# Kernel tuning notes

Hardware: AMD Instinct MI355X
Metric: run time of the kernel (lower is better)

Reference implementation:

```python
import jax, jax.numpy as jnp
import numpy as np

N_NODES = 100000
N_EDGES = 1600000
D_FEAT = 128
HIDDEN = 64
N_CLASSES = 40
NEG_SLOPE = 0.01  # jax.nn.leaky_relu default, matches flax nn.leaky_relu


def glorot(key, shape):
    fan_in, fan_out = shape
    return jax.random.normal(key, shape, dtype=jnp.float32) * jnp.sqrt(2.0 / (fan_in + fan_out))


def setup_inputs() -> dict:
    key = jax.random.key(0)
    ks = jax.random.split(key, 8)
    nodes = jax.random.normal(ks[0], (N_NODES, D_FEAT), dtype=jnp.float32)
    senders = jax.random.randint(ks[1], (N_EDGES,), 0, N_NODES, dtype=jnp.int32)
    receivers = jax.random.randint(ks[2], (N_EDGES,), 0, N_NODES, dtype=jnp.int32)
    W1 = glorot(ks[3], (D_FEAT, HIDDEN))
    b1 = jnp.zeros((HIDDEN,), jnp.float32)
    W2 = glorot(ks[4], (HIDDEN, HIDDEN))
    b2 = jnp.zeros((HIDDEN,), jnp.float32)
    W3 = glorot(ks[5], (HIDDEN, N_CLASSES))
    b3 = jnp.zeros((N_CLASSES,), jnp.float32)
    return {"nodes": nodes, "senders": senders, "receivers": receivers,
            "W1": W1, "b1": b1, "W2": W2, "b2": b2, "W3": W3, "b3": b3}


def gcn_aggregate(x, senders, receivers, n_nodes):
    """jraph.GraphConvolution symmetric_normalization aggregation (post update_node_fn)."""
    ones = jnp.ones(senders.shape[0], dtype=x.dtype)
    sender_deg = jax.ops.segment_sum(ones, senders, num_segments=n_nodes)
    receiver_deg = jax.ops.segment_sum(ones, receivers, num_segments=n_nodes)
    x = x * jax.lax.rsqrt(jnp.maximum(sender_deg, 1.0))[:, None]
    x = jax.ops.segment_sum(x[senders], receivers, num_segments=n_nodes)  # [N, F]
    x = x * jax.lax.rsqrt(jnp.maximum(receiver_deg, 1.0))[:, None]
    return x


def reference(nodes, senders, receivers, W1, b1, W2, b2, W3, b3):
    n = nodes.shape[0]
    # Layer 1: GraphConvolution(MLP([hidden, hidden], leaky_relu))
    h = jax.nn.leaky_relu(nodes @ W1 + b1, NEG_SLOPE)
    h = jax.nn.leaky_relu(h @ W2 + b2, NEG_SLOPE)
    h = gcn_aggregate(h, senders, receivers, n)
    # Dropout is deterministic (training=False) -> identity
    # Layer 2: GraphConvolution(Dense(number_classes))
    h = h @ W3 + b3
    h = gcn_aggregate(h, senders, receivers, n)
    return jax.nn.softmax(h, axis=-1)
```

## Files before the change

kernel.cpp:

```cpp
#include <hip/hip_runtime.h>
#include <hip/hip_fp16.h>

#define NEG_SLOPE 0.01f
#define RANGE_BITS 15
#define RANGE (1 << RANGE_BITS)
#define HWORDS (RANGE / 2)
#define SLICE_BITS 15
#define SLICE (1 << SLICE_BITS)

typedef _Float16 f16x8 __attribute__((ext_vector_type(8)));
typedef float f32x4 __attribute__((ext_vector_type(4)));

__device__ __forceinline__ float lrelu(float x) { return x > 0.f ? x : NEG_SLOPE * x; }

__device__ __forceinline__ unsigned pack2h(float a, float b) {
    __half2 h = __floats2half2_rn(a, b);
    unsigned u; __builtin_memcpy(&u, &h, 4); return u;
}
__device__ __forceinline__ float2 unpack2(unsigned u) {
    __half2 h = *reinterpret_cast<__half2*>(&u);
    return __half22float2(h);
}
__device__ __forceinline__ f16x8 u4h8(uint4 u) {
    f16x8 r; __builtin_memcpy(&r, &u, 16); return r;
}

__global__ __launch_bounds__(1024) void count_kernel(
    const int* __restrict__ snd, const int* __restrict__ rcv,
    unsigned* __restrict__ partial, unsigned short* __restrict__ pos16,
    int nE, int NR, int NS)
{
    __shared__ unsigned hist[HWORDS];
    const int b = blockIdx.x;
    const int a = b / (NR * NS);
    const int rem = b - a * NR * NS;
    const int r = rem / NS;
    const int s = rem - r * NS;
    const int t = threadIdx.x;
    for (int k = t; k < HWORDS; k += 1024) hist[k] = 0u;
    __syncthreads();
    const int base = r << RANGE_BITS;
    const int lo = s << SLICE_BITS;
    const int hi = min(lo + SLICE, nE);
    const int n4 = (hi - lo) >> 2;
    const int* arr = (a == 0) ? rcv : snd;
    const int4* arr4 = (const int4*)(arr + lo);
    if (a == 0) {
        for (int i4 = t; i4 < n4; i4 += 1024) {
            const int4 v = arr4[i4];
            const int ib = lo + i4 * 4;
            int vv[4] = {v.x, v.y, v.z, v.w};
#pragma unroll
            for (int c = 0; c < 4; ++c) {
                const unsigned d = (unsigned)(vv[c] - base);
                if (d < (unsigned)RANGE) {
                    const unsigned sh = (d & 1u) << 4;
                    const unsigned old = atomicAdd(&hist[d >> 1], 1u << sh);
                    pos16[ib + c] = (unsigned short)((old >> sh) & 0xffffu);
                }
            }
        }
        for (int i = lo + n4 * 4 + t; i < hi; i += 1024) {
            const unsigned d = (unsigned)(arr[i] - base);
            if (d < (unsigned)RANGE) {
                const unsigned sh = (d & 1u) << 4;
                const unsigned old = atomicAdd(&hist[d >> 1], 1u << sh);
                pos16[i] = (unsigned short)((old >> sh) & 0xffffu);
            }
        }
    } else {
        for (int i4 = t; i4 < n4; i4 += 1024) {
            const int4 v = arr4[i4];
            int vv[4] = {v.x, v.y, v.z, v.w};
#pragma unroll
            for (int c = 0; c < 4; ++c) {
                const unsigned d = (unsigned)(vv[c] - base);
                if (d < (unsigned)RANGE) atomicAdd(&hist[d >> 1], 1u << ((d & 1u) << 4));
            }
        }
        for (int i = lo + n4 * 4 + t; i < hi; i += 1024) {
            const unsigned d = (unsigned)(arr[i] - base);
            if (d < (unsigned)RANGE) atomicAdd(&hist[d >> 1], 1u << ((d & 1u) << 4));
        }
    }
    __syncthreads();
    unsigned* dst = partial + (size_t)((a * NR + r) * NS + s) * HWORDS;
    for (int k = t; k < HWORDS; k += 1024) dst[k] = hist[k];
}

__global__ __launch_bounds__(256) void scanp_kernel(
    unsigned* __restrict__ partial,
    int* __restrict__ dr_i,
    float* __restrict__ rin, float* __restrict__ rout,
    int nN, int NR, int NS)
{
    const int gid = blockIdx.x * 256 + threadIdx.x;
    if (gid >= NR * HWORDS) return;
    const int r  = gid >> (RANGE_BITS - 1);
    const int wd = gid & (HWORDS - 1);
    unsigned* prcv = partial + (size_t)(r * NS) * HWORDS + wd;
    unsigned run0 = 0, run1 = 0;
    for (int s = 0; s < NS; ++s) {
        unsigned* p = prcv + (size_t)s * HWORDS;
        const unsigned c = *p;
        *p = run0 | (run1 << 16);
        run0 += c & 0xffffu;
        run1 += c >> 16;
    }
    const unsigned* psnd = partial + (size_t)((NR + r) * NS) * HWORDS + wd;
    unsigned t0 = 0, t1 = 0;
    for (int s = 0; s < NS; ++s) {
        const unsigned c = psnd[(size_t)s * HWORDS];
        t0 += c & 0xffffu;
        t1 += c >> 16;
    }
    const int n0 = (r << RANGE_BITS) + 2 * wd;
    if (n0 < nN) {
        dr_i[n0] = (int)run0;
        rout[n0] = rsqrtf(fmaxf((float)run0, 1.f));
        rin[n0]  = rsqrtf(fmaxf((float)t0, 1.f));
    }
    if (n0 + 1 < nN) {
        dr_i[n0 + 1] = (int)run1;
        rout[n0 + 1] = rsqrtf(fmaxf((float)run1, 1.f));
        rin[n0 + 1]  = rsqrtf(fmaxf((float)t1, 1.f));
    }
}

__global__ __launch_bounds__(256) void scan1_kernel(const int* __restrict__ cnt,
                                                    int* __restrict__ rowptr,
                                                    int* __restrict__ bsums, int n)
{
    __shared__ int sd[256];
    const int t = threadIdx.x;
    const int base = blockIdx.x * 1024 + t * 4;
    int v0 = (base + 0 < n) ? cnt[base + 0] : 0;
    int v1 = (base + 1 < n) ? cnt[base + 1] : 0;
    int v2 = (base + 2 < n) ? cnt[base + 2] : 0;
    int v3 = (base + 3 < n) ? cnt[base + 3] : 0;
    const int p1 = v0, p2 = v0 + v1, p3 = v0 + v1 + v2;
    const int tot = p3 + v3;
    sd[t] = tot;
    __syncthreads();
    for (int off = 1; off < 256; off <<= 1) {
        int y = (t >= off) ? sd[t - off] : 0;
        __syncthreads();
        sd[t] += y;
        __syncthreads();
    }
    const int excl = sd[t] - tot;
    if (base + 0 < n) rowptr[base + 0] = excl;
    if (base + 1 < n) rowptr[base + 1] = excl + p1;
    if (base + 2 < n) rowptr[base + 2] = excl + p2;
    if (base + 3 < n) rowptr[base + 3] = excl + p3;
    if (t == 255) bsums[blockIdx.x] = sd[255];
}

__global__ __launch_bounds__(256) void scan2_kernel(int* __restrict__ bsums, int nb)
{
    __shared__ int sd[256];
    const int t = threadIdx.x;
    const int v = (t < nb) ? bsums[t] : 0;
    sd[t] = v;
    __syncthreads();
    for (int off = 1; off < 256; off <<= 1) {
        int y = (t >= off) ? sd[t - off] : 0;
        __syncthreads();
        sd[t] += y;
        __syncthreads();
    }
    if (t < nb) bsums[t] = sd[t] - v;
}

__global__ __launch_bounds__(256) void scan3_kernel(int* __restrict__ rowptr,
                                                    const int* __restrict__ bsums,
                                                    int n, int nE)
{
    const int gid = blockIdx.x * 256 + threadIdx.x;
    if (gid < n) rowptr[gid] += bsums[gid >> 10];
    if (gid == 0) rowptr[n] = nE;
}

__global__ __launch_bounds__(256) void fill_kernel(
    const int* __restrict__ snd, const int* __restrict__ rcv,
    const unsigned short* __restrict__ pos16, const unsigned* __restrict__ partial,
    const int* __restrict__ rowptr, int* __restrict__ csr_src,
    int nE, int NS)
{
    const int i = blockIdx.x * 256 + threadIdx.x;
    if (i >= nE) return;
    const int rv = rcv[i];
    const int r = rv >> RANGE_BITS;
    const int s = i >> SLICE_BITS;
    const unsigned pw = partial[(size_t)(r * NS + s) * HWORDS + ((rv & (RANGE - 1)) >> 1)];
    const int pref = (int)((pw >> ((rv & 1) << 4)) & 0xffffu);
    const int pos = rowptr[rv] + pref + (int)pos16[i];
    csr_src[pos] = snd[i];
}

__global__ __launch_bounds__(256) void mlp_kernel(
    const float* __restrict__ X, const float* __restrict__ W1, const float* __restrict__ b1,
    const float* __restrict__ W2, const float* __restrict__ b2, const float* __restrict__ W3,
    const float* __restrict__ rin, __half* __restrict__ p, int nN)
{
    __shared__ uint4 R1[1024];
    __shared__ uint4 R2[512];

    const int t    = threadIdx.x;
    const int w    = t >> 6;
    const int l    = t & 63;
    const int lrow = l & 15;
    const int lq   = l >> 4;
    const int row0 = blockIdx.x * 64;

    {
        const int c = l;
        for (int ch = 0; ch < 4; ++ch) {
            const int kc = 4 * w + ch;
            const float* wp = W1 + (kc * 8) * 64 + c;
            uint4 u;
            u.x = pack2h(wp[0],       wp[64]);
            u.y = pack2h(wp[2 * 64],  wp[3 * 64]);
            u.z = pack2h(wp[4 * 64],  wp[5 * 64]);
            u.w = pack2h(wp[6 * 64],  wp[7 * 64]);
            R1[c * 16 + (kc ^ (c & 7))] = u;
        }
    }
    __syncthreads();

    const int grow = row0 + 16 * w + lrow;
    const bool rowok = grow < nN;
    const float* xr = X + (size_t)grow * 128 + lq * 8;

    f32x4 acc1[4];
#pragma unroll
    for (int nt = 0; nt < 4; ++nt) acc1[nt] = (f32x4){0.f, 0.f, 0.f, 0.f};

#pragma unroll
    for (int ks = 0; ks < 4; ++ks) {
        float4 xa = make_float4(0.f, 0.f, 0.f, 0.f), xb = xa;
        if (rowok) {
            xa = *(const float4*)(xr + 32 * ks);
            xb = *(const float4*)(xr + 32 * ks + 4);
        }
        uint4 au;
        au.x = pack2h(xa.x, xa.y); au.y = pack2h(xa.z, xa.w);
        au.z = pack2h(xb.x, xb.y); au.w = pack2h(xb.z, xb.w);
        const f16x8 af = u4h8(au);
        const int kc = 4 * ks + lq;
#pragma unroll
        for (int nt = 0; nt < 4; ++nt) {
            const int c = 16 * nt + lrow;
            const uint4 bu = R1[c * 16 + (kc ^ (c & 7))];
            acc1[nt] = __builtin_amdgcn_mfma_f32_16x16x32_f16(af, u4h8(bu), acc1[nt], 0, 0, 0);
        }
    }
    __syncthreads();

    {
        __half* hh = (__half*)R2;
#pragma unroll
        for (int nt = 0; nt < 4; ++nt) {
            const int col = 16 * nt + lrow;
            const float bv = b1[col];
            const int ch = col >> 3, cl = col & 7;
#pragma unroll
            for (int r = 0; r < 4; ++r) {
                const int rw = 16 * w + 4 * lq + r;
                hh[rw * 64 + ((ch ^ (rw & 7)) * 8) + cl] = __float2half(lrelu(acc1[nt][r] + bv));
            }
        }
        const int c = l;
#pragma unroll
        for (int ch = 0; ch < 2; ++ch) {
            const int kc = 2 * w + ch;
            const float* wp = W2 + (kc * 8) * 64 + c;
            uint4 u;
            u.x = pack2h(wp[0],      wp[64]);
            u.y = pack2h(wp[2 * 64], wp[3 * 64]);
            u.z = pack2h(wp[4 * 64], wp[5 * 64]);
            u.w = pack2h(wp[6 * 64], wp[7 * 64]);
            R1[c * 8 + (kc ^ (c & 7))] = u;
        }
        if (c < 48) {
            const bool cv = c < 40;
#pragma unroll
            for (int ch = 0; ch < 2; ++ch) {
                const int kc = 2 * w + ch;
                const float* wp = W3 + (kc * 8) * 40 + c;
                uint4 u;
                u.x = pack2h(cv ? wp[0]      : 0.f, cv ? wp[40]     : 0.f);
                u.y = pack2h(cv ? wp[2 * 40] : 0.f, cv ? wp[3 * 40] : 0.f);
                u.z = pack2h(cv ? wp[4 * 40] : 0.f, cv ? wp[5 * 40] : 0.f);
                u.w = pack2h(cv ? wp[6 * 40] : 0.f, cv ? wp[7 * 40] : 0.f);
                R1[512 + c * 8 + (kc ^ (c & 7))] = u;
            }
        }
    }
    __syncthreads();

    f32x4 acc2[4];
#pragma unroll
    for (int nt = 0; nt < 4; ++nt) acc2[nt] = (f32x4){0.f, 0.f, 0.f, 0.f};
    {
        const int ar = 16 * w + lrow;
#pragma unroll
        for (int ks = 0; ks < 2; ++ks) {
            const int kc = 4 * ks + lq;
            const f16x8 af = u4h8(R2[ar * 8 + (kc ^ (ar & 7))]);
#pragma unroll
            for (int nt = 0; nt < 4; ++nt) {
                const int c = 16 * nt + lrow;
                const uint4 bu = R1[c * 8 + (kc ^ (c & 7))];
                acc2[nt] = __builtin_amdgcn_mfma_f32_16x16x32_f16(af, u4h8(bu), acc2[nt], 0, 0, 0);
            }
        }
    }
    __syncthreads();

    {
        __half* hh = (__half*)R2;
#pragma unroll
        for (int nt = 0; nt < 4; ++nt) {
            const int col = 16 * nt + lrow;
            const float bv = b2[col];
            const int ch = col >> 3, cl = col & 7;
#pragma unroll
            for (int r = 0; r < 4; ++r) {
                const int rw = 16 * w + 4 * lq + r;
                hh[rw * 64 + ((ch ^ (rw & 7)) * 8) + cl] = __float2half(lrelu(acc2[nt][r] + bv));
            }
        }
    }
    __syncthreads();

    f32x4 acc3[3];
#pragma unroll
    for (int nt = 0; nt < 3; ++nt) acc3[nt] = (f32x4){0.f, 0.f, 0.f, 0.f};
    {
        const int ar = 16 * w + lrow;
#pragma unroll
        for (int ks = 0; ks < 2; ++ks) {
            const int kc = 4 * ks + lq;
            const f16x8 af = u4h8(R2[ar * 8 + (kc ^ (ar & 7))]);
#pragma unroll
            for (int nt = 0; nt < 3; ++nt) {
                const int c = 16 * nt + lrow;
                const uint4 bu = R1[512 + c * 8 + (kc ^ (c & 7))];
                acc3[nt] = __builtin_amdgcn_mfma_f32_16x16x32_f16(af, u4h8(bu), acc3[nt], 0, 0, 0);
            }
        }
    }

#pragma unroll
    for (int r = 0; r < 4; ++r) {
        const int gr = row0 + 16 * w + 4 * lq + r;
        if (gr < nN) {
            const float rs = rin[gr];
            __half* pr = p + (size_t)gr * 40;
#pragma unroll
            for (int nt = 0; nt < 3; ++nt) {
                const int col = 16 * nt + lrow;
                if (col < 40) pr[col] = __float2half(acc3[nt][r] * rs);
            }
        }
    }
}

__global__ __launch_bounds__(256) void agg1_kernel(const __half* __restrict__ p,
                                                   const int* __restrict__ csr_src,
                                                   const int* __restrict__ rowptr,
                                                   const float* __restrict__ rin,
                                                   const float* __restrict__ rout,
                                                   __half* __restrict__ qbuf,
                                                   float* __restrict__ cbuf, int nN)
{
    const int gid = blockIdx.x * 256 + threadIdx.x;
    const int node = gid >> 3;
    const int j = gid & 7;
    if (node >= nN) return;
    const int beg = rowptr[node], end = rowptr[node + 1];
    const bool isch = (j < 5);
    const bool isr  = (j == 5);
    float a[8];
#pragma unroll
    for (int k = 0; k < 8; ++k) a[k] = 0.f;
    float cs = 0.f;

    for (int e = beg; e < end; e += 8) {
        int s[8];
#pragma unroll
        for (int b = 0; b < 8; ++b) {
            const int idx = e + b;
            s[b] = csr_src[idx < end ? idx : end - 1];
        }
        if (isch) {
            uint4 u[8];
#pragma unroll
            for (int b = 0; b < 8; ++b)
                u[b] = ((const uint4*)(p + (size_t)s[b] * 40))[j];
#pragma unroll
            for (int b = 0; b < 8; ++b) {
                if (e + b < end) {
                    float2 f;
                    f = unpack2(u[b].x); a[0] += f.x; a[1] += f.y;
                    f = unpack2(u[b].y); a[2] += f.x; a[3] += f.y;
                    f = unpack2(u[b].z); a[4] += f.x; a[5] += f.y;
                    f = unpack2(u[b].w); a[6] += f.x; a[7] += f.y;
                }
            }
        } else if (isr) {
            float rr[8];
#pragma unroll
            for (int b = 0; b < 8; ++b) rr[b] = rin[s[b]];
#pragma unroll
            for (int b = 0; b < 8; ++b)
                if (e + b < end) cs += rr[b];
        }
    }

    if (isch) {
        const float sc = rin[node] * rout[node];
        uint4 o;
        o.x = pack2h(a[0] * sc, a[1] * sc);
        o.y = pack2h(a[2] * sc, a[3] * sc);
        o.z = pack2h(a[4] * sc, a[5] * sc);
        o.w = pack2h(a[6] * sc, a[7] * sc);
        ((uint4*)(qbuf + (size_t)node * 40))[j] = o;
    } else if (isr) {
        cbuf[node] = cs * rout[node];
    }
}

__global__ __launch_bounds__(256) void agg2_kernel(const __half* __restrict__ qbuf,
                                                   const int* __restrict__ csr_src,
                                                   const int* __restrict__ rowptr,
                                                   const float* __restrict__ rout,
                                                   const float* __restrict__ cbuf,
                                                   const float* __restrict__ b3,
                                                   float* __restrict__ out, int nN)
{
    const int gid = blockIdx.x * 256 + threadIdx.x;
    const int node = gid >> 3;
    const int j = gid & 7;
    if (node >= nN) return;
    const int beg = rowptr[node], end = rowptr[node + 1];
    const bool isch = (j < 5);
    float a[8];
#pragma unroll
    for (int k = 0; k < 8; ++k) a[k] = 0.f;

    for (int e = beg; e < end; e += 8) {
        int s[8];
#pragma unroll
        for (int b = 0; b < 8; ++b) {
            const int idx = e + b;
            s[b] = csr_src[idx < end ? idx : end - 1];
        }
        if (isch) {
            uint4 u[8];
#pragma unroll
            for (int b = 0; b < 8; ++b)
                u[b] = ((const uint4*)(qbuf + (size_t)s[b] * 40))[j];
#pragma unroll
            for (int b = 0; b < 8; ++b) {
                if (e + b < end) {
                    float2 f;
                    f = unpack2(u[b].x); a[0] += f.x; a[1] += f.y;
                    f = unpack2(u[b].y); a[2] += f.x; a[3] += f.y;
                    f = unpack2(u[b].z); a[4] += f.x; a[5] += f.y;
                    f = unpack2(u[b].w); a[6] += f.x; a[7] += f.y;
                }
            }
        }
    }

    const float ro = rout[node];
    const float c  = cbuf[node];
    float z[8];
    float m = -1e30f, ssum = 0.f;
    if (isch) {
#pragma unroll
        for (int k = 0; k < 8; ++k) {
            z[k] = ro * a[k] + c * b3[j * 8 + k];
            m = fmaxf(m, z[k]);
        }
    }
    m = fmaxf(m, __shfl_xor(m, 1));
    m = fmaxf(m, __shfl_xor(m, 2));
    m = fmaxf(m, __shfl_xor(m, 4));
    if (isch) {
#pragma unroll
        for (int k = 0; k < 8; ++k) { z[k] = __expf(z[k] - m); ssum += z[k]; }
    }
    ssum += __shfl_xor(ssum, 1);
    ssum += __shfl_xor(ssum, 2);
    ssum += __shfl_xor(ssum, 4);
    if (isch) {
        const float inv = 1.f / ssum;
        float4* orow = (float4*)(out + (size_t)node * 40);
        orow[j * 2 + 0] = make_float4(z[0] * inv, z[1] * inv, z[2] * inv, z[3] * inv);
        orow[j * 2 + 1] = make_float4(z[4] * inv, z[5] * inv, z[6] * inv, z[7] * inv);
    }
}

extern "C" void kernel_launch(void* const* d_in, const int* in_sizes, int n_in,
                              void* d_out, int out_size, void* d_ws, size_t ws_size,
                              hipStream_t stream)
{
    const float* nodes = (const float*)d_in[0];
    const int*   snd   = (const int*)d_in[1];
    const int*   rcv   = (const int*)d_in[2];
    const float* W1    = (const float*)d_in[3];
    const float* b1    = (const float*)d_in[4];
    const float* W2    = (const float*)d_in[5];
    const float* b2    = (const float*)d_in[6];
    const float* W3    = (const float*)d_in[7];
    const float* b3    = (const float*)d_in[8];

    const int nN = in_sizes[0] / 128;
    const int nE = in_sizes[1];
    const int NR = (nN + RANGE - 1) >> RANGE_BITS;
    const int NS = (nE + SLICE - 1) >> SLICE_BITS;
    const int nb1 = (nN + 1023) / 1024;

    size_t off = 0;
    auto alloc = [&](size_t n) { size_t r = off; off += (n + 3) & ~(size_t)3; return r; };
    int*   dr_i    = (int*)d_ws + alloc(nN);
    int*   rowptr  = (int*)d_ws + alloc(nN + 1);
    int*   bsums   = (int*)d_ws + alloc(256);
    float* rin     = (float*)d_ws + alloc(nN);
    float* rout    = (float*)d_ws + alloc(nN);
    float* cbuf    = (float*)d_ws + alloc(nN);
    int*   csr_src = (int*)d_ws + alloc(nE);
    const size_t psz = (size_t)2 * NR * NS * HWORDS;
    size_t ubase = alloc(0);
    unsigned*       partial = (unsigned*)d_ws + ubase;
    unsigned short* pos16   = (unsigned short*)((unsigned*)d_ws + ubase + psz);
    __half* pbuf = (__half*)((int*)d_ws + ubase);
    __half* qbuf = pbuf + (size_t)nN * 40;

    count_kernel<<<2 * NR * NS, 1024, 0, stream>>>(snd, rcv, partial, pos16, nE, NR, NS);
    scanp_kernel<<<(NR * HWORDS + 255) / 256, 256, 0, stream>>>(partial, dr_i, rin, rout, nN, NR, NS);
    scan1_kernel<<<nb1, 256, 0, stream>>>(dr_i, rowptr, bsums, nN);
    scan2_kernel<<<1, 256, 0, stream>>>(bsums, nb1);
    scan3_kernel<<<(nN + 255) / 256, 256, 0, stream>>>(rowptr, bsums, nN, nE);
    fill_kernel<<<(nE + 255) / 256, 256, 0, stream>>>(snd, rcv, pos16, partial, rowptr, csr_src, nE, NS);
    mlp_kernel<<<(nN + 63) / 64, 256, 0, stream>>>(nodes, W1, b1, W2, b2, W3, rin, pbuf, nN);
    agg1_kernel<<<((size_t)nN * 8 + 255) / 256, 256, 0, stream>>>(pbuf, csr_src, rowptr, rin, rout, qbuf, cbuf, nN);
    agg2_kernel<<<((size_t)nN * 8 + 255) / 256, 256, 0, stream>>>(qbuf, csr_src, rowptr, rout, cbuf, b3, (float*)d_out, nN);
}
```

Baseline: 172.5 us.

## Split second aggregation into feature-column passes with a separate softmax kernel

The layer-2 gather is split into three passes, each reading a narrower column slice of the fp16 feature table (16, 16 and 8 halves per node). Each slice is small enough to stay resident in cache, which should improve hit rates on the random gathers. Partial logits go to an fp32 staging buffer and a new per-node softmax kernel reads them back. The cost is rereading the CSR indices three times, extra launches, and extra global traffic for the staging buffer. SLICE_BITS also changes from 15 to 16, which alters the partitioning of the degree-count and CSR-build kernels.

After: 195.8 us. +13.5%, slower.

```diff
diff --git a/kernel.cpp b/kernel.cpp
--- a/kernel.cpp
+++ b/kernel.cpp
@@ -5,7 +5,7 @@
 #define RANGE_BITS 15
 #define RANGE (1 << RANGE_BITS)
 #define HWORDS (RANGE / 2)
-#define SLICE_BITS 15
+#define SLICE_BITS 16
 #define SLICE (1 << SLICE_BITS)
 
 typedef _Float16 f16x8 __attribute__((ext_vector_type(8)));
@@ -372,7 +372,9 @@
                                                    const int* __restrict__ rowptr,
                                                    const float* __restrict__ rin,
                                                    const float* __restrict__ rout,
-                                                   __half* __restrict__ qbuf,
+                                                   __half* __restrict__ qA,
+                                                   __half* __restrict__ qB,
+                                                   __half* __restrict__ qC,
                                                    float* __restrict__ cbuf, int nN)
 {
     const int gid = blockIdx.x * 256 + threadIdx.x;
@@ -426,26 +428,29 @@
         o.y = pack2h(a[2] * sc, a[3] * sc);
         o.z = pack2h(a[4] * sc, a[5] * sc);
         o.w = pack2h(a[6] * sc, a[7] * sc);
-        ((uint4*)(qbuf + (size_t)node * 40))[j] = o;
+        if (j < 2)      ((uint4*)qA)[(size_t)node * 2 + j] = o;
+        else if (j < 4) ((uint4*)qB)[(size_t)node * 2 + (j - 2)] = o;
+        else            ((uint4*)qC)[node] = o;
     } else if (isr) {
         cbuf[node] = cs * rout[node];
     }
 }
 
-__global__ __launch_bounds__(256) void agg2_kernel(const __half* __restrict__ qbuf,
-                                                   const int* __restrict__ csr_src,
-                                                   const int* __restrict__ rowptr,
-                                                   const float* __restrict__ rout,
-                                                   const float* __restrict__ cbuf,
-                                                   const float* __restrict__ b3,
-                                                   float* __restrict__ out, int nN)
+template <int LPN>
+__global__ __launch_bounds__(256) void agg2_pass_kernel(const __half* __restrict__ qsub,
+                                                        const int* __restrict__ csr_src,
+                                                        const int* __restrict__ rowptr,
+                                                        const float* __restrict__ rout,
+                                                        const float* __restrict__ cbuf,
+                                                        const float* __restrict__ b3,
+                                                        float* __restrict__ zbuf,
+                                                        int chbase, int nN)
 {
     const int gid = blockIdx.x * 256 + threadIdx.x;
-    const int node = gid >> 3;
-    const int j = gid & 7;
+    const int node = (LPN == 2) ? (gid >> 1) : gid;
+    const int j    = (LPN == 2) ? (gid & 1) : 0;
     if (node >= nN) return;
     const int beg = rowptr[node], end = rowptr[node + 1];
-    const bool isch = (j < 5);
     float a[8];
 #pragma unroll
     for (int k = 0; k < 8; ++k) a[k] = 0.f;
@@ -457,51 +462,64 @@
             const int idx = e + b;
             s[b] = csr_src[idx < end ? idx : end - 1];
         }
-        if (isch) {
-            uint4 u[8];
-#pragma unroll
-            for (int b = 0; b < 8; ++b)
-                u[b] = ((const uint4*)(qbuf + (size_t)s[b] * 40))[j];
-#pragma unroll
-            for (int b = 0; b < 8; ++b) {
-                if (e + b < end) {
-                    float2 f;
-                    f = unpack2(u[b].x); a[0] += f.x; a[1] += f.y;
-                    f = unpack2(u[b].y); a[2] += f.x; a[3] += f.y;
-                    f = unpack2(u[b].z); a[4] += f.x; a[5] += f.y;
-                    f = unpack2(u[b].w); a[6] += f.x; a[7] += f.y;
-                }
+        uint4 u[8];
+#pragma unroll
+        for (int b = 0; b < 8; ++b)
+            u[b] = ((const uint4*)qsub)[(size_t)s[b] * LPN + j];
+#pragma unroll
+        for (int b = 0; b < 8; ++b) {
+            if (e + b < end) {
+                float2 f;
+                f = unpack2(u[b].x); a[0] += f.x; a[1] += f.y;
+                f = unpack2(u[b].y); a[2] += f.x; a[3] += f.y;
+                f = unpack2(u[b].z); a[4] += f.x; a[5] += f.y;
+                f = unpack2(u[b].w); a[6] += f.x; a[7] += f.y;
             }
         }
     }
 
     const float ro = rout[node];
     const float c  = cbuf[node];
-    float z[8];
-    float m = -1e30f, ssum = 0.f;
-    if (isch) {
-#pragma unroll
-        for (int k = 0; k < 8; ++k) {
-            z[k] = ro * a[k] + c * b3[j * 8 + k];
-            m = fmaxf(m, z[k]);
-        }
-    }
-    m = fmaxf(m, __shfl_xor(m, 1));
-    m = fmaxf(m, __shfl_xor(m, 2));
-    m = fmaxf(m, __shfl_xor(m, 4));
-    if (isch) {
-#pragma unroll
-        for (int k = 0; k < 8; ++k) { z[k] = __expf(z[k] - m); ssum += z[k]; }
-    }
-    ssum += __shfl_xor(ssum, 1);
-    ssum += __shfl_xor(ssum, 2);
-    ssum += __shfl_xor(ssum, 4);
-    if (isch) {
-        const float inv = 1.f / ssum;
-        float4* orow = (float4*)(out + (size_t)node * 40);
-        orow[j * 2 + 0] = make_float4(z[0] * inv, z[1] * inv, z[2] * inv, z[3] * inv);
-        orow[j * 2 + 1] = make_float4(z[4] * inv, z[5] * inv, z[6] * inv, z[7] * inv);
-    }
+    const int ch = chbase + j;
+    float4 z0, z1;
+    z0.x = ro * a[0] + c * b3[ch * 8 + 0];
+    z0.y = ro * a[1] + c * b3[ch * 8 + 1];
+    z0.z = ro * a[2] + c * b3[ch * 8 + 2];
+    z0.w = ro * a[3] + c * b3[ch * 8 + 3];
+    z1.x = ro * a[4] + c * b3[ch * 8 + 4];
+    z1.y = ro * a[5] + c * b3[ch * 8 + 5];
+    z1.z = ro * a[6] + c * b3[ch * 8 + 6];
+    z1.w = ro * a[7] + c * b3[ch * 8 + 7];
+    float4* zp = (float4*)zbuf + ((size_t)ch * nN + node) * 2;
+    zp[0] = z0;
+    zp[1] = z1;
+}
+
+__global__ __launch_bounds__(256) void softmax_kernel(const float* __restrict__ zbuf,
+                                                      float* __restrict__ out, int nN)
+{
+    const int node = blockIdx.x * 256 + threadIdx.x;
+    if (node >= nN) return;
+    float v[40];
+#pragma unroll
+    for (int c = 0; c < 5; ++c) {
+        const float4* zp = (const float4*)zbuf + ((size_t)c * nN + node) * 2;
+        const float4 a = zp[0], b = zp[1];
+        v[c * 8 + 0] = a.x; v[c * 8 + 1] = a.y; v[c * 8 + 2] = a.z; v[c * 8 + 3] = a.w;
+        v[c * 8 + 4] = b.x; v[c * 8 + 5] = b.y; v[c * 8 + 6] = b.z; v[c * 8 + 7] = b.w;
+    }
+    float m = v[0];
+#pragma unroll
+    for (int c = 1; c < 40; ++c) m = fmaxf(m, v[c]);
+    float s = 0.f;
+#pragma unroll
+    for (int c = 0; c < 40; ++c) { v[c] = __expf(v[c] - m); s += v[c]; }
+    const float inv = 1.f / s;
+    float4* orow = (float4*)(out + (size_t)node * 40);
+#pragma unroll
+    for (int c4 = 0; c4 < 10; ++c4)
+        orow[c4] = make_float4(v[c4 * 4 + 0] * inv, v[c4 * 4 + 1] * inv,
+                               v[c4 * 4 + 2] * inv, v[c4 * 4 + 3] * inv);
 }
 
 extern "C" void kernel_launch(void* const* d_in, const int* in_sizes, int n_in,
@@ -538,7 +556,10 @@
     unsigned*       partial = (unsigned*)d_ws + ubase;
     unsigned short* pos16   = (unsigned short*)((unsigned*)d_ws + ubase + psz);
     __half* pbuf = (__half*)((int*)d_ws + ubase);
-    __half* qbuf = pbuf + (size_t)nN * 40;
+    __half* qA   = pbuf + (size_t)nN * 40;
+    __half* qB   = qA + (size_t)nN * 16;
+    __half* qC   = qB + (size_t)nN * 16;
+    float*  zbuf = (float*)(qC + (size_t)nN * 8);
 
     count_kernel<<<2 * NR * NS, 1024, 0, stream>>>(snd, rcv, partial, pos16, nE, NR, NS);
     scanp_kernel<<<(NR * HWORDS + 255) / 256, 256, 0, stream>>>(partial, dr_i, rin, rout, nN, NR, NS);
@@ -547,6 +568,9 @@
     scan3_kernel<<<(nN + 255) / 256, 256, 0, stream>>>(rowptr, bsums, nN, nE);
     fill_kernel<<<(nE + 255) / 256, 256, 0, stream>>>(snd, rcv, pos16, partial, rowptr, csr_src, nE, NS);
     mlp_kernel<<<(nN + 63) / 64, 256, 0, stream>>>(nodes, W1, b1, W2, b2, W3, rin, pbuf, nN);
-    agg1_kernel<<<((size_t)nN * 8 + 255) / 256, 256, 0, stream>>>(pbuf, csr_src, rowptr, rin, rout, qbuf, cbuf, nN);
-    agg2_kernel<<<((size_t)nN * 8 + 255) / 256, 256, 0, stream>>>(qbuf, csr_src, rowptr, rout, cbuf, b3, (float*)d_out, nN);
-}
+    agg1_kernel<<<((size_t)nN * 8 + 255) / 256, 256, 0, stream>>>(pbuf, csr_src, rowptr, rin, rout, qA, qB, qC, cbuf, nN);
+    agg2_pass_kernel<2><<<((size_t)nN * 2 + 255) / 256, 256, 0, stream>>>(qA, csr_src, rowptr, rout, cbuf, b3, zbuf, 0, nN);
+    agg2_pass_kernel<2><<<((size_t)nN * 2 + 255) / 256, 256, 0, stream>>>(qB, csr_src, rowptr, rout, cbuf, b3, zbuf, 2, nN);
+    agg2_pass_kernel<1><<<((size_t)nN + 255) / 256, 256, 0, stream>>>(qC, csr_src, rowptr, rout, cbuf, b3, zbuf, 4, nN);
+    softmax_kernel<<<(nN + 255) / 256, 256, 0, stream>>>(zbuf, (float*)d_out, nN);
+}
```
